# Kernel optimization log

Measured on AMD Instinct MI355X. Metric: run time of the kernel, lower is better.

The kernel has to match this reference:

```python
import jax, jax.numpy as jnp
import numpy as np

BETA = 0.25

def setup_inputs() -> dict:
    key = jax.random.key(0)
    k1, k2 = jax.random.split(key)
    N, D, K = 262144, 64, 512
    encoding = jax.random.normal(k1, (N, D), dtype=jnp.float32)
    # original inits uniform(-1/K, 1/K); scale a normal similarly is fine, but stay faithful:
    weight = jax.random.uniform(k2, (K, D), dtype=jnp.float32, minval=-1.0 / K, maxval=1.0 / K)
    return {"encoding": encoding, "weight": weight}


def reference(encoding, weight):
    # flat view: encoding already [N, D]
    x = encoding  # [N, D]
    # squared euclidean distances; argmin is invariant to sqrt and to ||x||^2 term
    x2 = jnp.sum(x * x, axis=1, keepdims=True)            # [N, 1]
    w2 = jnp.sum(weight * weight, axis=1)                  # [K]
    d2 = x2 - 2.0 * (x @ weight.T) + w2[None, :]           # [N, K]
    idx = jnp.argmin(d2, axis=1)                           # [N]
    quantized = weight[idx]                                # gather == one_hot @ weight, [N, D]

    commitment_loss = jnp.mean((jax.lax.stop_gradient(quantized) - x) ** 2)
    embedding_loss = jnp.mean((quantized - jax.lax.stop_gradient(x)) ** 2)
    vq_loss = commitment_loss * BETA + embedding_loss

    # straight-through estimator
    quantized_st = x + jax.lax.stop_gradient(quantized - x)
    return (idx[:, None], quantized_st, vq_loss)
```

## Files before the change

kernel.cpp:

```cpp
#include <hip/hip_runtime.h>

#define NROWS 262144
#define DDIM  64
#define KCB   512

#define MARGKEY (3u << 17)

#define WS_CNT   0
#define WS_W2P3  1024
#define WS_WHI   4096
#define WS_WMID  69632
#define WS_LIST  135168

typedef __attribute__((ext_vector_type(8))) short short8;
typedef __attribute__((ext_vector_type(4))) float floatx4;
typedef __attribute__((ext_vector_type(16))) float floatx16;
typedef __attribute__((ext_vector_type(2))) unsigned int uintx2;

#if defined(__has_builtin)
#if __has_builtin(__builtin_amdgcn_permlane32_swap)
#define VQ_PLSWAP 1
#endif
#endif

__device__ __forceinline__ unsigned umin2(unsigned a, unsigned b) { return a < b ? a : b; }
__device__ __forceinline__ unsigned umax2(unsigned a, unsigned b) { return a > b ? a : b; }

__device__ __forceinline__ float np_sumsq64(const float* a) {
    float r[8];
#pragma unroll
    for (int j = 0; j < 8; ++j) r[j] = __fmul_rn(a[j], a[j]);
#pragma unroll
    for (int i = 8; i < 64; i += 8) {
#pragma unroll
        for (int j = 0; j < 8; ++j)
            r[j] = __fadd_rn(r[j], __fmul_rn(a[i + j], a[i + j]));
    }
    return __fadd_rn(__fadd_rn(__fadd_rn(r[0], r[1]), __fadd_rn(r[2], r[3])),
                     __fadd_rn(__fadd_rn(r[4], r[5]), __fadd_rn(r[6], r[7])));
}

__device__ __forceinline__ void split2(float e0, float e1, unsigned& hid, unsigned& mid) {
    unsigned u0 = __float_as_uint(e0), u1 = __float_as_uint(e1);
    float r0 = __fsub_rn(e0, __uint_as_float(u0 & 0xFFFF0000u));
    float r1 = __fsub_rn(e1, __uint_as_float(u1 & 0xFFFF0000u));
    hid = (u0 >> 16) | (u1 & 0xFFFF0000u);
    mid = (__float_as_uint(r0) >> 16) | (__float_as_uint(r1) & 0xFFFF0000u);
}

__device__ __forceinline__ void split4(float4 v, uint2& h, uint2& m) {
    unsigned h0, m0, h1, m1;
    split2(v.x, v.y, h0, m0);
    split2(v.z, v.w, h1, m1);
    h = make_uint2(h0, h1);
    m = make_uint2(m0, m1);
}

__device__ __forceinline__ void merge32(unsigned& m1, unsigned& m2) {
#ifdef VQ_PLSWAP
    uintx2 s1 = __builtin_amdgcn_permlane32_swap(m1, m1, false, false);
    uintx2 s2 = __builtin_amdgcn_permlane32_swap(m2, m2, false, false);
    m2 = umin2(umin2(s2[0], s2[1]), umax2(s1[0], s1[1]));
    m1 = umin2(s1[0], s1[1]);
#else
    unsigned o1 = __shfl_xor((int)m1, 32);
    unsigned o2 = __shfl_xor((int)m2, 32);
    m2 = umin2(umin2(m2, o2), umax2(m1, o1));
    m1 = umin2(m1, o1);
#endif
}

__device__ __forceinline__ void top2_16(const unsigned* k, unsigned& m1, unsigned& m2) {
    unsigned lo[8], hi[8];
#pragma unroll
    for (int i = 0; i < 8; ++i) {
        lo[i] = umin2(k[2 * i], k[2 * i + 1]);
        hi[i] = umax2(k[2 * i], k[2 * i + 1]);
    }
#pragma unroll
    for (int s = 4; s >= 1; s >>= 1) {
#pragma unroll
        for (int i = 0; i < s; ++i) {
            unsigned l = umin2(lo[i], lo[i + s]);
            unsigned h = umin2(umax2(lo[i], lo[i + s]), umin2(hi[i], hi[i + s]));
            lo[i] = l; hi[i] = h;
        }
    }
    m1 = lo[0]; m2 = hi[0];
}

__global__ void vq_prep(const float* __restrict__ w, float* __restrict__ w2p3,
                        unsigned short* __restrict__ whi,
                        unsigned short* __restrict__ wmid,
                        unsigned* __restrict__ cnt, float* __restrict__ loss) {
    const int k = blockIdx.x * blockDim.x + threadIdx.x;
    if (k == 0) { *cnt = 0u; *loss = 0.0f; }
    float ws[64];
    const float4* wp = (const float4*)(w + (size_t)k * DDIM);
#pragma unroll
    for (int j = 0; j < 16; ++j) {
        float4 v = wp[j];
        ws[4 * j + 0] = v.x; ws[4 * j + 1] = v.y;
        ws[4 * j + 2] = v.z; ws[4 * j + 3] = v.w;
    }
    w2p3[k] = __fadd_rn(np_sumsq64(ws), 3.0f);
#pragma unroll
    for (int j = 0; j < 8; ++j) {
        union { unsigned d[4]; short8 s; } H, M;
#pragma unroll
        for (int t = 0; t < 4; ++t) {
            float v0 = __fmul_rn(-2.0f, ws[8 * j + 2 * t]);
            float v1 = __fmul_rn(-2.0f, ws[8 * j + 2 * t + 1]);
            split2(v0, v1, H.d[t], M.d[t]);
        }
        *(short8*)(whi  + (size_t)k * 64 + 8 * j) = H.s;
        *(short8*)(wmid + (size_t)k * 64 + 8 * j) = M.s;
    }
}

__launch_bounds__(256, 4)
__global__ void vq_gemm(const float* __restrict__ x,
                        const unsigned short* __restrict__ whi,
                        const unsigned short* __restrict__ wmid,
                        const float* __restrict__ w2p3g,
                        uint2* __restrict__ mmg) {
    const int tid = threadIdx.x;
    const int wave = tid >> 6, lane = tid & 63;
    const int row32 = lane & 31;
    const int khalf = lane >> 5;
    const int half = blockIdx.x & 1;
    const int r0 = (blockIdx.x >> 1) * 256;

    __shared__ float w2p3s[256];
    __shared__ __align__(16) unsigned sbh[2][32 * 36];
    __shared__ __align__(16) unsigned sbm[2][32 * 36];
    __shared__ uint2 mm[4][8][32];

    w2p3s[tid] = w2p3g[half * 256 + tid];

    short8 ah[2][4], am[2][4];
#pragma unroll
    for (int tt = 0; tt < 2; ++tt) {
        const size_t cw = (size_t)(half * 256 + wave * 64 + tt * 32 + row32);
#pragma unroll
        for (int t = 0; t < 4; ++t) {
            const size_t off = cw * 64 + t * 16 + khalf * 8;
            ah[tt][t] = *(const short8*)(whi + off);
            am[tt][t] = *(const short8*)(wmid + off);
        }
    }

    const int srow = tid >> 4, sc4 = tid & 15;
    {
        float4 v0 = *(const float4*)(x + (size_t)(r0 + srow) * DDIM + 4 * sc4);
        float4 v1 = *(const float4*)(x + (size_t)(r0 + srow + 16) * DDIM + 4 * sc4);
        uint2 h, m;
        split4(v0, h, m);
        *(uint2*)&sbh[0][srow * 36 + 2 * sc4] = h;
        *(uint2*)&sbm[0][srow * 36 + 2 * sc4] = m;
        split4(v1, h, m);
        *(uint2*)&sbh[0][(srow + 16) * 36 + 2 * sc4] = h;
        *(uint2*)&sbm[0][(srow + 16) * 36 + 2 * sc4] = m;
    }
    __syncthreads();

    const unsigned cwk = (unsigned)(half * 256 + wave * 64 + 4 * khalf);

    for (int it = 0; it < 8; ++it) {
        const int p = it & 1;
        float4 pre0, pre1;
        if (it < 7) {
            pre0 = *(const float4*)(x + (size_t)(r0 + (it + 1) * 32 + srow) * DDIM + 4 * sc4);
            pre1 = *(const float4*)(x + (size_t)(r0 + (it + 1) * 32 + srow + 16) * DDIM + 4 * sc4);
        }

        short8 bh[4], bm[4];
#pragma unroll
        for (int t = 0; t < 4; ++t) {
            bh[t] = *(const short8*)&sbh[p][row32 * 36 + t * 8 + khalf * 4];
            bm[t] = *(const short8*)&sbm[p][row32 * 36 + t * 8 + khalf * 4];
        }

        unsigned r1t[2], r2t[2];
#pragma unroll
        for (int tt = 0; tt < 2; ++tt) {
            floatx16 acc;
            const int wb = wave * 64 + tt * 32 + 4 * khalf;
#pragma unroll
            for (int g = 0; g < 4; ++g) {
                floatx4 v = *(const floatx4*)&w2p3s[wb + 8 * g];
                acc[4 * g + 0] = v[0]; acc[4 * g + 1] = v[1];
                acc[4 * g + 2] = v[2]; acc[4 * g + 3] = v[3];
            }
#pragma unroll
            for (int t = 0; t < 4; ++t) {
                acc = __builtin_amdgcn_mfma_f32_32x32x16_bf16(ah[tt][t], bh[t], acc, 0, 0, 0);
                acc = __builtin_amdgcn_mfma_f32_32x32x16_bf16(ah[tt][t], bm[t], acc, 0, 0, 0);
                acc = __builtin_amdgcn_mfma_f32_32x32x16_bf16(am[tt][t], bh[t], acc, 0, 0, 0);
            }
            unsigned keys[16];
#pragma unroll
            for (int r = 0; r < 16; ++r) {
                const unsigned moff = (unsigned)((r & 3) + 8 * (r >> 2) + tt * 32);
                keys[r] = (__float_as_uint(acc[r]) << 9) + cwk + moff;
            }
            top2_16(keys, r1t[tt], r2t[tt]);
        }
        unsigned m1 = umin2(r1t[0], r1t[1]);
        unsigned m2 = umin2(umax2(r1t[0], r1t[1]), umin2(r2t[0], r2t[1]));
        merge32(m1, m2);
        if (lane < 32) mm[wave][it][row32] = make_uint2(m1, m2);

        if (it < 7) {
            uint2 h, m;
            split4(pre0, h, m);
            *(uint2*)&sbh[p ^ 1][srow * 36 + 2 * sc4] = h;
            *(uint2*)&sbm[p ^ 1][srow * 36 + 2 * sc4] = m;
            split4(pre1, h, m);
            *(uint2*)&sbh[p ^ 1][(srow + 16) * 36 + 2 * sc4] = h;
            *(uint2*)&sbm[p ^ 1][(srow + 16) * 36 + 2 * sc4] = m;
        }
        __syncthreads();
    }

    unsigned a1 = 0xFFFFFFFFu, a2 = 0xFFFFFFFFu;
#pragma unroll
    for (int wv = 0; wv < 4; ++wv) {
        uint2 v = mm[wv][tid >> 5][tid & 31];
        a2 = umin2(umin2(a2, v.y), umax2(a1, v.x));
        a1 = umin2(a1, v.x);
    }
    mmg[(size_t)half * NROWS + (r0 + tid)] = make_uint2(a1, a2);
}

__launch_bounds__(256)
__global__ void vq_merge(const uint2* __restrict__ mmg,
                         float* __restrict__ out_idx,
                         unsigned* __restrict__ cnt,
                         unsigned* __restrict__ list, int listcap) {
    const int row = blockIdx.x * 256 + threadIdx.x;
    const int lane = threadIdx.x & 63;
    uint2 v0 = mmg[row];
    uint2 v1 = mmg[(size_t)NROWS + row];
    unsigned a1 = umin2(v0.x, v1.x);
    unsigned a2 = umin2(umax2(v0.x, v1.x), umin2(v0.y, v1.y));
    out_idx[row] = (float)(a1 & 511u);
    bool flag = (a2 - a1 < MARGKEY);
    unsigned long long mask = __ballot(flag);
    int nw = __popcll(mask);
    unsigned base = 0;
    if (lane == 0 && nw) base = atomicAdd(cnt, (unsigned)nw);
    base = (unsigned)__shfl((int)base, 0);
    if (flag) {
        unsigned pos = base + (unsigned)__popcll(mask & ((1ull << lane) - 1ull));
        if ((int)pos < listcap) list[pos] = (unsigned)row;
    }
}

__launch_bounds__(512, 4)
__global__ void vq_recheck(const float* __restrict__ x,
                           const float* __restrict__ w,
                           const unsigned* __restrict__ cnt,
                           const unsigned* __restrict__ list, int listcap,
                           float* __restrict__ out_idx) {
    const int tid = threadIdx.x;
    unsigned total = *cnt;
    if (total > (unsigned)listcap) total = (unsigned)listcap;
    const unsigned nb = (total + 15) >> 4;
    if (blockIdx.x >= nb) return;

    float wl[64];
    {
        const float4* wp = (const float4*)(w + (size_t)tid * DDIM);
#pragma unroll
        for (int j = 0; j < 16; ++j) {
            float4 v = wp[j];
            wl[4 * j + 0] = v.x; wl[4 * j + 1] = v.y;
            wl[4 * j + 2] = v.z; wl[4 * j + 3] = v.w;
        }
    }
    const float w2l = np_sumsq64(wl);

    __shared__ float d2tile[16][KCB];
    __shared__ int rowbuf[16];
    __shared__ float x2buf[16];

    for (unsigned batch = blockIdx.x; batch < nb; batch += gridDim.x) {
        if (tid < 16) {
            unsigned li = batch * 16 + (unsigned)tid;
            rowbuf[tid] = (li < total) ? (int)list[li] : -1;
        }
        __syncthreads();

        if (tid < 128) {
            const int rl = tid >> 3, j = tid & 7;
            int row = rowbuf[rl]; if (row < 0) row = 0;
            const float* xr = x + (size_t)row * DDIM;
            float a0 = xr[j];
            float r = __fmul_rn(a0, a0);
#pragma unroll
            for (int i = 1; i < 8; ++i) {
                float ai = xr[8 * i + j];
                r = __fadd_rn(r, __fmul_rn(ai, ai));
            }
            float s1 = __fadd_rn(r,  __shfl_xor(r, 1));
            float s2 = __fadd_rn(s1, __shfl_xor(s1, 2));
            float s4 = __fadd_rn(s2, __shfl_xor(s2, 4));
            if (j == 0) x2buf[rl] = s4;
        }
        __syncthreads();

        for (int g = 0; g < 16; g += 4) {
            int ra = rowbuf[g + 0]; if (ra < 0) ra = 0;
            int rb = rowbuf[g + 1]; if (rb < 0) rb = 0;
            int rc = rowbuf[g + 2]; if (rc < 0) rc = 0;
            int rd = rowbuf[g + 3]; if (rd < 0) rd = 0;
            const float* xr0 = x + (size_t)ra * DDIM;
            const float* xr1 = x + (size_t)rb * DDIM;
            const float* xr2 = x + (size_t)rc * DDIM;
            const float* xr3 = x + (size_t)rd * DDIM;
            float m0 = 0.f, m1 = 0.f, m2 = 0.f, m3 = 0.f;
#pragma unroll
            for (int jb = 0; jb < 16; ++jb) {
                float4 a0 = *(const float4*)(xr0 + 4 * jb);
                float4 a1 = *(const float4*)(xr1 + 4 * jb);
                float4 a2 = *(const float4*)(xr2 + 4 * jb);
                float4 a3 = *(const float4*)(xr3 + 4 * jb);
                m0 = __fmaf_rn(a0.x, wl[4 * jb + 0], m0);
                m0 = __fmaf_rn(a0.y, wl[4 * jb + 1], m0);
                m0 = __fmaf_rn(a0.z, wl[4 * jb + 2], m0);
                m0 = __fmaf_rn(a0.w, wl[4 * jb + 3], m0);
                m1 = __fmaf_rn(a1.x, wl[4 * jb + 0], m1);
                m1 = __fmaf_rn(a1.y, wl[4 * jb + 1], m1);
                m1 = __fmaf_rn(a1.z, wl[4 * jb + 2], m1);
                m1 = __fmaf_rn(a1.w, wl[4 * jb + 3], m1);
                m2 = __fmaf_rn(a2.x, wl[4 * jb + 0], m2);
                m2 = __fmaf_rn(a2.y, wl[4 * jb + 1], m2);
                m2 = __fmaf_rn(a2.z, wl[4 * jb + 2], m2);
                m2 = __fmaf_rn(a2.w, wl[4 * jb + 3], m2);
                m3 = __fmaf_rn(a3.x, wl[4 * jb + 0], m3);
                m3 = __fmaf_rn(a3.y, wl[4 * jb + 1], m3);
                m3 = __fmaf_rn(a3.z, wl[4 * jb + 2], m3);
                m3 = __fmaf_rn(a3.w, wl[4 * jb + 3], m3);
            }
            float X0 = x2buf[g + 0], X1 = x2buf[g + 1];
            float X2 = x2buf[g + 2], X3 = x2buf[g + 3];
            d2tile[g + 0][tid] = __fadd_rn(__fsub_rn(X0, __fmul_rn(2.0f, m0)), w2l);
            d2tile[g + 1][tid] = __fadd_rn(__fsub_rn(X1, __fmul_rn(2.0f, m1)), w2l);
            d2tile[g + 2][tid] = __fadd_rn(__fsub_rn(X2, __fmul_rn(2.0f, m2)), w2l);
            d2tile[g + 3][tid] = __fadd_rn(__fsub_rn(X3, __fmul_rn(2.0f, m3)), w2l);
        }
        __syncthreads();

        {
            const int rl  = tid >> 5;
            const int sub = tid & 31;
            float bv = d2tile[rl][sub];
            int   bi = sub;
#pragma unroll
            for (int i = 1; i < 16; ++i) {
                int cc = sub + 32 * i;
                float v = d2tile[rl][cc];
                if (v < bv) { bv = v; bi = cc; }
            }
#pragma unroll
            for (int s = 1; s < 32; s <<= 1) {
                float ov = __shfl_xor(bv, s);
                int   oi = __shfl_xor(bi, s);
                if (ov < bv || (ov == bv && oi < bi)) { bv = ov; bi = oi; }
            }
            if (sub == 0 && rowbuf[rl] >= 0) out_idx[rowbuf[rl]] = (float)bi;
        }
        __syncthreads();
    }
}

__launch_bounds__(256)
__global__ void vq_epilogue(const float* __restrict__ x,
                            const float* __restrict__ w,
                            const float* __restrict__ out_idx_f,
                            float* __restrict__ out_q,
                            float* __restrict__ out_loss) {
    const int row  = blockIdx.x * blockDim.x + threadIdx.x;
    const int bidx = (int)out_idx_f[row];

    const float4* xp = (const float4*)(x + (size_t)row * DDIM);
    const float4* wq = (const float4*)(w + (size_t)bidx * DDIM);
    float4* qo = (float4*)(out_q + (size_t)row * DDIM);
    float ls = 0.0f;
#pragma unroll
    for (int j = 0; j < 16; ++j) {
        float4 xv = xp[j];
        float4 wv = wq[j];
        float e0 = __fsub_rn(wv.x, xv.x), e1 = __fsub_rn(wv.y, xv.y);
        float e2 = __fsub_rn(wv.z, xv.z), e3 = __fsub_rn(wv.w, xv.w);
        ls = fmaf(e0, e0, ls); ls = fmaf(e1, e1, ls);
        ls = fmaf(e2, e2, ls); ls = fmaf(e3, e3, ls);
        float4 q;
        q.x = __fadd_rn(xv.x, e0); q.y = __fadd_rn(xv.y, e1);
        q.z = __fadd_rn(xv.z, e2); q.w = __fadd_rn(xv.w, e3);
        qo[j] = q;
    }
#pragma unroll
    for (int off = 32; off > 0; off >>= 1) ls += __shfl_down(ls, off);
    __shared__ float red[4];
    const int lane = threadIdx.x & 63;
    const int wid  = threadIdx.x >> 6;
    if (lane == 0) red[wid] = ls;
    __syncthreads();
    if (threadIdx.x == 0) {
        float t = (red[0] + red[1]) + (red[2] + red[3]);
        atomicAdd(out_loss, t * (1.25f / (float)(NROWS * DDIM)));
    }
}

extern "C" void kernel_launch(void* const* d_in, const int* in_sizes, int n_in,
                              void* d_out, int out_size, void* d_ws, size_t ws_size,
                              hipStream_t stream) {
    const float* x = (const float*)d_in[0];
    const float* w = (const float*)d_in[1];

    float* out      = (float*)d_out;
    float* out_idx  = out;
    float* out_q    = out + (size_t)NROWS;
    float* out_loss = out + (size_t)NROWS + (size_t)NROWS * DDIM;

    uint2* mmg = (uint2*)out_q;

    char* ws = (char*)d_ws;
    unsigned* cnt  = (unsigned*)(ws + WS_CNT);
    float* w2p3    = (float*)(ws + WS_W2P3);
    unsigned short* whi  = (unsigned short*)(ws + WS_WHI);
    unsigned short* wmid = (unsigned short*)(ws + WS_WMID);
    unsigned* list = (unsigned*)(ws + WS_LIST);
    long cap = ((long)ws_size - WS_LIST) / 4;
    int listcap = cap > 0 ? (cap > NROWS ? NROWS : (int)cap) : 0;

    vq_prep<<<2, 256, 0, stream>>>(w, w2p3, whi, wmid, cnt, out_loss);
    vq_gemm<<<2048, 256, 0, stream>>>(x, whi, wmid, w2p3, mmg);
    vq_merge<<<NROWS / 256, 256, 0, stream>>>(mmg, out_idx, cnt, list, listcap);
    vq_recheck<<<256, 512, 0, stream>>>(x, w, cnt, list, listcap, out_idx);
    vq_epilogue<<<NROWS / 256, 256, 0, stream>>>(x, w, out_idx, out_q, out_loss);
}
```

Before: 261.2 us.

## Stage epilogue rows through LDS for coalesced I/O and raise MFMA priority

The epilogue now loads 128-row tiles of x into shared memory with a row-contiguous, coalesced pattern. Half the threads compute the quantized rows and the loss in place in the tile, and the tile is then written back coalesced. This replaces the old scheme where each thread streamed its own 256-byte row, which strided accesses across lanes. The distance kernel also wraps its MFMA chain in s_setprio(1)/s_setprio(0) to favour issuing matrix instructions. The trade-offs are extra barriers, only half the threads busy in the compute phase, and float4 LDS accesses on a 65-float padded stride that are not 16-byte aligned.

New measurement: 282.7 us. +8.2%, slower.

```diff
diff --git a/kernel.cpp b/kernel.cpp
--- a/kernel.cpp
+++ b/kernel.cpp
@@ -192,12 +192,14 @@
                 acc[4 * g + 0] = v[0]; acc[4 * g + 1] = v[1];
                 acc[4 * g + 2] = v[2]; acc[4 * g + 3] = v[3];
             }
+            __builtin_amdgcn_s_setprio(1);
 #pragma unroll
             for (int t = 0; t < 4; ++t) {
                 acc = __builtin_amdgcn_mfma_f32_32x32x16_bf16(ah[tt][t], bh[t], acc, 0, 0, 0);
                 acc = __builtin_amdgcn_mfma_f32_32x32x16_bf16(ah[tt][t], bm[t], acc, 0, 0, 0);
                 acc = __builtin_amdgcn_mfma_f32_32x32x16_bf16(am[tt][t], bh[t], acc, 0, 0, 0);
             }
+            __builtin_amdgcn_s_setprio(0);
             unsigned keys[16];
 #pragma unroll
             for (int r = 0; r < 16; ++r) {
@@ -381,34 +383,60 @@
                             const float* __restrict__ out_idx_f,
                             float* __restrict__ out_q,
                             float* __restrict__ out_loss) {
-    const int row  = blockIdx.x * blockDim.x + threadIdx.x;
-    const int bidx = (int)out_idx_f[row];
-
-    const float4* xp = (const float4*)(x + (size_t)row * DDIM);
+    const int tid = threadIdx.x;
+    const int r0  = blockIdx.x * 256;
+    const int bidx = (int)out_idx_f[r0 + tid];
     const float4* wq = (const float4*)(w + (size_t)bidx * DDIM);
-    float4* qo = (float4*)(out_q + (size_t)row * DDIM);
+
+    __shared__ float tile[128][65];
+    __shared__ float red[4];
+
     float ls = 0.0f;
 #pragma unroll
-    for (int j = 0; j < 16; ++j) {
-        float4 xv = xp[j];
-        float4 wv = wq[j];
-        float e0 = __fsub_rn(wv.x, xv.x), e1 = __fsub_rn(wv.y, xv.y);
-        float e2 = __fsub_rn(wv.z, xv.z), e3 = __fsub_rn(wv.w, xv.w);
-        ls = fmaf(e0, e0, ls); ls = fmaf(e1, e1, ls);
-        ls = fmaf(e2, e2, ls); ls = fmaf(e3, e3, ls);
-        float4 q;
-        q.x = __fadd_rn(xv.x, e0); q.y = __fadd_rn(xv.y, e1);
-        q.z = __fadd_rn(xv.z, e2); q.w = __fadd_rn(xv.w, e3);
-        qo[j] = q;
-    }
+    for (int ph = 0; ph < 2; ++ph) {
+        const int rb = r0 + ph * 128;
+        __syncthreads();
+#pragma unroll
+        for (int i = 0; i < 8; ++i) {
+            const int li = tid + 256 * i;
+            const int row = li >> 4, c4 = li & 15;
+            float4 v = *(const float4*)(x + (size_t)(rb + row) * DDIM + 4 * c4);
+            *(float4*)&tile[row][4 * c4] = v;
+        }
+        __syncthreads();
+        if ((tid >> 7) == ph) {
+            const int lr = tid & 127;
+#pragma unroll
+            for (int j = 0; j < 16; ++j) {
+                float4 xv = *(const float4*)&tile[lr][4 * j];
+                float4 wv = wq[j];
+                float e0 = __fsub_rn(wv.x, xv.x), e1 = __fsub_rn(wv.y, xv.y);
+                float e2 = __fsub_rn(wv.z, xv.z), e3 = __fsub_rn(wv.w, xv.w);
+                ls = fmaf(e0, e0, ls); ls = fmaf(e1, e1, ls);
+                ls = fmaf(e2, e2, ls); ls = fmaf(e3, e3, ls);
+                float4 q;
+                q.x = __fadd_rn(xv.x, e0); q.y = __fadd_rn(xv.y, e1);
+                q.z = __fadd_rn(xv.z, e2); q.w = __fadd_rn(xv.w, e3);
+                *(float4*)&tile[lr][4 * j] = q;
+            }
+        }
+        __syncthreads();
+#pragma unroll
+        for (int i = 0; i < 8; ++i) {
+            const int li = tid + 256 * i;
+            const int row = li >> 4, c4 = li & 15;
+            float4 qv = *(const float4*)&tile[row][4 * c4];
+            *(float4*)(out_q + (size_t)(rb + row) * DDIM + 4 * c4) = qv;
+        }
+    }
+
 #pragma unroll
     for (int off = 32; off > 0; off >>= 1) ls += __shfl_down(ls, off);
-    __shared__ float red[4];
-    const int lane = threadIdx.x & 63;
-    const int wid  = threadIdx.x >> 6;
+    const int lane = tid & 63;
+    const int wid  = tid >> 6;
     if (lane == 0) red[wid] = ls;
     __syncthreads();
-    if (threadIdx.x == 0) {
+    if (tid == 0) {
         float t = (red[0] + red[1]) + (red[2] + red[3]);
         atomicAdd(out_loss, t * (1.25f / (float)(NROWS * DDIM)));
     }
```
